# Optimization experiments

Hardware: AMD Instinct MI355X
Metric: run time of the kernel (lower is better)

## Reference

```python
import jax, jax.numpy as jnp
import numpy as np

B, N, P = 8, 64, 128
DNODE, DEDGE, DEMB = 2048, 1024, 512
E = B * N * N


def setup_inputs() -> dict:
    key = jax.random.key(0)
    ks = jax.random.split(key, 12)
    x = jax.random.normal(ks[0], (B, N, DNODE), dtype=jnp.float32)
    interaction_feature = jax.random.normal(ks[1], (B, N, N, DEDGE), dtype=jnp.float32)
    s = 0.02
    W_phi = jax.random.normal(ks[2], (DNODE, DEMB), dtype=jnp.float32) * s
    b_phi = jax.random.normal(ks[3], (DEMB,), dtype=jnp.float32) * s
    W_psi = jax.random.normal(ks[4], (DNODE, DEMB), dtype=jnp.float32) * s
    b_psi = jax.random.normal(ks[5], (DEMB,), dtype=jnp.float32) * s
    W_node = jax.random.normal(ks[6], (DNODE, DEMB), dtype=jnp.float32) * s
    b_node = jax.random.normal(ks[7], (DEMB,), dtype=jnp.float32) * s
    W_rel = jax.random.normal(ks[8], (DEDGE, DEMB), dtype=jnp.float32) * s
    b_rel = jax.random.normal(ks[9], (DEMB,), dtype=jnp.float32) * s
    pairs = jax.random.randint(ks[10], (B, P, 2), 0, N, dtype=jnp.int32)
    # edge_locating_tensor: rows (batch, src, dst) covering the proposed edge set
    bb, ii, jj = jnp.meshgrid(jnp.arange(B), jnp.arange(N), jnp.arange(N), indexing='ij')
    edge_locating_tensor = jnp.stack([bb.ravel(), ii.ravel(), jj.ravel()], axis=1).astype(jnp.int32)  # [E,3]
    return {"x": x, "interaction_feature": interaction_feature, "W_phi": W_phi, "b_phi": b_phi,
            "W_psi": W_psi, "b_psi": b_psi, "W_node": W_node, "b_node": b_node,
            "W_rel": W_rel, "b_rel": b_rel, "pairs": pairs, "edge_locating_tensor": edge_locating_tensor}


def _lookup_edge(elt, b_idx, i0, i1):
    # boolean-mask argmax lookup, faithful to torch argmax(loc0*loc1*loc2)
    # elt: [E,3]; b_idx,i0,i1: [B,P] -> loc: [B,P] indices into edge list
    m = (elt[None, None, :, 0] == b_idx[:, :, None]) \
        & (elt[None, None, :, 1] == i0[:, :, None]) \
        & (elt[None, None, :, 2] == i1[:, :, None])  # [B,P,E]
    return jnp.argmax(m, axis=-1)


def reference(x, interaction_feature, W_phi, b_phi, W_psi, b_psi,
              W_node, b_node, W_rel, b_rel, pairs, edge_locating_tensor):
    # relationship proposal scoring: all-pairs einsum + sigmoid
    phi = x @ W_phi + b_phi                                    # [B,N,512]
    psi = x @ W_psi + b_psi                                    # [B,N,512]
    relatedness_score = jax.nn.sigmoid(jnp.einsum('bik,bjk->bij', phi, psi))  # [B,N,N]

    # node / relationship-node embedders
    node_emb = x @ W_node + b_node                             # [B,N,512]
    elt = edge_locating_tensor
    rel_feats = interaction_feature[elt[:, 0], elt[:, 1], elt[:, 2]]  # [E,1024] gather
    edge_emb = rel_feats @ W_rel + b_rel                       # [E,512]

    # classifier input construction (gather/argmax/scatter hot path, vectorized)
    ind0, ind1 = pairs[..., 0], pairs[..., 1]                  # [B,P]
    b_idx = jnp.broadcast_to(jnp.arange(B, dtype=jnp.int32)[:, None], ind0.shape)
    emb0 = node_emb[b_idx, ind0]                               # [B,P,512]
    emb1 = node_emb[b_idx, ind1]
    first_half = (emb0 + emb1) * 0.5                           # aggregate 'mean'

    loc_fwd = _lookup_edge(elt, b_idx, ind0, ind1)             # [B,P]
    loc_rev = _lookup_edge(elt, b_idx, ind1, ind0)
    e1 = edge_emb[loc_fwd]                                     # [B,P,512]
    e2 = edge_emb[loc_rev]
    second_half = (e1 + e2) * 0.5

    classifier_input = jnp.concatenate([first_half, second_half], axis=-1)  # [B,P,1024]
    return relatedness_score, classifier_input
```

## Files before the change

### kernel.cpp

```cpp
#include <hip/hip_runtime.h>
#include <hip/hip_bf16.h>


typedef _Float16 h16;
typedef h16 h16x4 __attribute__((ext_vector_type(4)));
typedef h16 h16x8 __attribute__((ext_vector_type(8)));
typedef float f32x4 __attribute__((ext_vector_type(4)));

static const long O_W3T  = 0;
static const long O_WREL = 6291456;
static const long O_XH   = 7340032;
static const long O_G    = 9437184;
static const long O_B3   = 11534336;
static const long O_YH   = 11540480;

__global__ __launch_bounds__(256) void k_prep(
    const float* __restrict__ Wphi, const float* __restrict__ Wpsi,
    const float* __restrict__ Wnode, const float* __restrict__ Wrel,
    const float* __restrict__ x, const float* __restrict__ bphi,
    const float* __restrict__ bpsi, const float* __restrict__ bnode,
    const float* __restrict__ feat, const int* __restrict__ pairs,
    h16* __restrict__ W3t, h16* __restrict__ Wrelt, h16* __restrict__ xh,
    float* __restrict__ b3, h16* __restrict__ G) {
  __shared__ float t[32][33];
  int bid = blockIdx.x, tid = threadIdx.x;
  if (bid < 3584) {
    const float* src; h16* dst; int K, tk, tn;
    if (bid < 3072) {
      int mat = bid >> 10, rem = bid & 1023;
      tk = rem >> 4; tn = rem & 15;
      src = mat == 0 ? Wphi : (mat == 1 ? Wpsi : Wnode);
      K = 2048; dst = W3t + (long)mat * 512 * 2048;
    } else {
      int rem = bid - 3072;
      tk = rem >> 4; tn = rem & 15;
      src = Wrel; K = 1024; dst = Wrelt;
    }
    {
      int row = tid >> 3, c4 = (tid & 7) * 4;
      float4 v = *(const float4*)(src + (long)(tk*32 + row)*512 + tn*32 + c4);
      t[row][c4+0] = v.x; t[row][c4+1] = v.y; t[row][c4+2] = v.z; t[row][c4+3] = v.w;
    }
    __syncthreads();
    {
      int n = tid >> 3, k4 = (tid & 7) * 4;
      h16x4 o = { (h16)t[k4+0][n], (h16)t[k4+1][n], (h16)t[k4+2][n], (h16)t[k4+3][n] };
      *(h16x4*)(dst + (long)(tn*32 + n)*K + tk*32 + k4) = o;
    }
  } else if (bid < 4102) {
    int b2 = bid - 3584;
    if (b2 < 512) {
      int idx = (b2*256 + tid) * 8;
      const float4* xv = (const float4*)(x + idx);
      float4 v0 = xv[0], v1 = xv[1];
      h16x8 o;
      o[0]=(h16)v0.x; o[1]=(h16)v0.y; o[2]=(h16)v0.z; o[3]=(h16)v0.w;
      o[4]=(h16)v1.x; o[5]=(h16)v1.y; o[6]=(h16)v1.z; o[7]=(h16)v1.w;
      *(h16x8*)(xh + idx) = o;
    } else {
      int i = (b2 - 512)*256 + tid;
      if (i < 1536) b3[i] = i < 512 ? bphi[i] : (i < 1024 ? bpsi[i-512] : bnode[i-1024]);
    }
  } else {
    int r = bid - 4102;
    int b = r >> 7;
    int i0 = pairs[r*2], i1 = pairs[r*2+1];
    const float4* f0 = (const float4*)(feat + (long)((b*64 + i0)*64 + i1) * 1024);
    const float4* f1 = (const float4*)(feat + (long)((b*64 + i1)*64 + i0) * 1024);
    float4 a = f0[tid], c = f1[tid];
    h16x4 o;
    o[0]=(h16)(0.5f*(a.x+c.x)); o[1]=(h16)(0.5f*(a.y+c.y));
    o[2]=(h16)(0.5f*(a.z+c.z)); o[3]=(h16)(0.5f*(a.w+c.w));
    *(h16x4*)(G + (long)r*1024 + tid*4) = o;
  }
}

__device__ __forceinline__ void mfma4(
    const h16 (*__restrict__ As)[72], const h16 (*__restrict__ Bs)[72],
    int wm, int wn, int kb, int fr, f32x4 acc[2][2]) {
  h16x8 fa0 = *(const h16x8*)&As[wm*32 + fr][kb];
  h16x8 fa1 = *(const h16x8*)&As[wm*32 + 16 + fr][kb];
  h16x8 fb0 = *(const h16x8*)&Bs[wn*32 + fr][kb];
  h16x8 fb1 = *(const h16x8*)&Bs[wn*32 + 16 + fr][kb];
  acc[0][0] = __builtin_amdgcn_mfma_f32_16x16x32_f16(fa0, fb0, acc[0][0], 0,0,0);
  acc[0][1] = __builtin_amdgcn_mfma_f32_16x16x32_f16(fa0, fb1, acc[0][1], 0,0,0);
  acc[1][0] = __builtin_amdgcn_mfma_f32_16x16x32_f16(fa1, fb0, acc[1][0], 0,0,0);
  acc[1][1] = __builtin_amdgcn_mfma_f32_16x16x32_f16(fa1, fb1, acc[1][1], 0,0,0);
}

#define BAR_LDS() { asm volatile("s_waitcnt lgkmcnt(0)" ::: "memory"); \
                    __builtin_amdgcn_s_barrier(); }

template<int S>
__device__ __forceinline__ void tile_splitk(
    const h16* Agp, const h16* Bgp,
    h16 (*As)[64][72], h16 (*Bs)[64][72],
    int srow, int skp, int wm, int wn, int kb, int fr,
    f32x4 acc[2][2]) {
  h16x8 r0a = *(const h16x8*)(Agp);
  h16x8 r0b = *(const h16x8*)(Bgp);
  *(h16x8*)&As[0][srow][skp] = r0a;
  *(h16x8*)&Bs[0][srow][skp] = r0b;
  h16x8 ra1 = *(const h16x8*)(Agp + 64),  rb1 = *(const h16x8*)(Bgp + 64);
  h16x8 ra2 = *(const h16x8*)(Agp + 128), rb2 = *(const h16x8*)(Bgp + 128);
  BAR_LDS();
  int cur = 0;
#pragma unroll 1
  for (int k0 = 192; k0 < S * 64; k0 += 64) {
    h16x8 raF = *(const h16x8*)(Agp + k0);
    h16x8 rbF = *(const h16x8*)(Bgp + k0);
    mfma4(As[cur], Bs[cur], wm, wn, kb, fr, acc);
    *(h16x8*)&As[cur ^ 1][srow][skp] = ra1;
    *(h16x8*)&Bs[cur ^ 1][srow][skp] = rb1;
    BAR_LDS();
    ra1 = ra2; rb1 = rb2; ra2 = raF; rb2 = rbF;
    cur ^= 1;
  }
  mfma4(As[cur], Bs[cur], wm, wn, kb, fr, acc);
  *(h16x8*)&As[cur ^ 1][srow][skp] = ra1;
  *(h16x8*)&Bs[cur ^ 1][srow][skp] = rb1;
  BAR_LDS();
  cur ^= 1;
  mfma4(As[cur], Bs[cur], wm, wn, kb, fr, acc);
  *(h16x8*)&As[cur ^ 1][srow][skp] = ra2;
  *(h16x8*)&Bs[cur ^ 1][srow][skp] = rb2;
  BAR_LDS();
  cur ^= 1;
  mfma4(As[cur], Bs[cur], wm, wn, kb, fr, acc);
}

__device__ __forceinline__ void splitk_merge(
    h16 (*As)[64][72], int wave, int lane, f32x4 acc[2][2]) {
  float* mb = (float*)As;
  __syncthreads();
  if (wave >= 4) {
    int mi = ((wave - 4) * 64 + lane) * 16;
    *(f32x4*)&mb[mi +  0] = acc[0][0];
    *(f32x4*)&mb[mi +  4] = acc[0][1];
    *(f32x4*)&mb[mi +  8] = acc[1][0];
    *(f32x4*)&mb[mi + 12] = acc[1][1];
  }
  __syncthreads();
  if (wave < 4) {
    int mi = (wave * 64 + lane) * 16;
    acc[0][0] += *(const f32x4*)&mb[mi +  0];
    acc[0][1] += *(const f32x4*)&mb[mi +  4];
    acc[1][0] += *(const f32x4*)&mb[mi +  8];
    acc[1][1] += *(const f32x4*)&mb[mi + 12];
  }
}

__global__ __launch_bounds__(512) void k_gemm(
    const h16* __restrict__ xh, const h16* __restrict__ W3t,
    const float* __restrict__ b3, h16* __restrict__ Yh,
    const h16* __restrict__ G, const h16* __restrict__ Wrelt,
    const float* __restrict__ brel, float* __restrict__ out) {
  __shared__ __align__(16) h16 As[2][64][72];
  __shared__ __align__(16) h16 Bs[2][64][72];
  int bid = blockIdx.x, tid = threadIdx.x;
  int lane = tid & 63, wave = tid >> 6;
  int kslice = wave >> 2, wsub = wave & 3;
  int wm = wsub >> 1, wn = wsub & 1;
  int srow = tid >> 3, skp = (tid & 7) * 8;
  int fr = lane & 15, kb = kslice * 32 + (lane >> 4) * 8;
  int r0 = 4 * (lane >> 4), c0 = lane & 15;

  int isEdge = bid >= 192;
  int ntile = isEdge ? 2 : 1;
#pragma unroll 1
  for (int ti = 0; ti < ntile; ++ti) {
    if (ti) __syncthreads();
    const h16 *A, *Bt; int K, tileM, tileN;
    if (!isEdge) {
      A = xh; Bt = W3t; K = 2048;
      tileM = (bid / 24) * 64; tileN = (bid % 24) * 64;
    } else {
      int e = (bid - 192) * 2 + ti;
      A = G; Bt = Wrelt; K = 1024;
      tileM = (e >> 3) * 64; tileN = (e & 7) * 64;
    }
    const h16* Agp = A + (long)(tileM + srow) * K + skp;
    const h16* Bgp = Bt + (long)(tileN + srow) * K + skp;
    f32x4 acc[2][2] = {};
    if (!isEdge) tile_splitk<32>(Agp, Bgp, As, Bs, srow, skp, wm, wn, kb, fr, acc);
    else         tile_splitk<16>(Agp, Bgp, As, Bs, srow, skp, wm, wn, kb, fr, acc);
    splitk_merge(As, wave, lane, acc);

    if (wave < 4) {
#pragma unroll
      for (int m = 0; m < 2; ++m)
#pragma unroll
        for (int n = 0; n < 2; ++n) {
          int row = tileM + wm*32 + m*16 + r0;
          int col = tileN + wn*32 + n*16 + c0;
          if (!isEdge) {
            float bb = b3[col];
#pragma unroll
            for (int r = 0; r < 4; ++r)
              Yh[(long)(row + r) * 1536 + col] = (h16)(acc[m][n][r] + bb);
          } else {
            float bb = brel[col];
#pragma unroll
            for (int r = 0; r < 4; ++r)
              out[32768 + 512 + (long)(row + r) * 1024 + col] = acc[m][n][r] + bb;
          }
        }
    }
  }
}

__global__ __launch_bounds__(512) void k_epilogue(
    const h16* __restrict__ Yh, const int* __restrict__ pairs,
    float* __restrict__ out) {
  __shared__ __align__(16) h16 As[2][64][72];
  __shared__ __align__(16) h16 Bs[2][64][72];
  int bid = blockIdx.x, tid = threadIdx.x;
  if (bid < 8) {
    int lane = tid & 63, wave = tid >> 6;
    int kslice = wave >> 2, wsub = wave & 3;
    int wm = wsub >> 1, wn = wsub & 1;
    int srow = tid >> 3, skp = (tid & 7) * 8;
    int fr = lane & 15, kb = kslice * 32 + (lane >> 4) * 8;
    const h16* Ab = Yh + (long)bid * 64 * 1536;
    const h16* Agp = Ab + (long)srow * 1536 + skp;
    const h16* Bgp = Ab + (long)srow * 1536 + 512 + skp;
    f32x4 acc[2][2] = {};
    tile_splitk<8>(Agp, Bgp, As, Bs, srow, skp, wm, wn, kb, fr, acc);
    splitk_merge(As, wave, lane, acc);
    if (wave < 4) {
      int r0 = 4 * (lane >> 4), c0 = lane & 15;
      float* ob = out + (long)bid * 4096;
#pragma unroll
      for (int m = 0; m < 2; ++m)
#pragma unroll
        for (int n = 0; n < 2; ++n) {
          int row = wm*32 + m*16 + r0;
          int col = wn*32 + n*16 + c0;
#pragma unroll
          for (int r = 0; r < 4; ++r) {
            float s = acc[m][n][r];
            ob[(long)(row + r) * 64 + col] = 1.f / (1.f + expf(-s));
          }
        }
    }
  } else {
    int r = bid - 8;
    int b = r >> 7;
    int i0 = pairs[r*2], i1 = pairs[r*2+1];
    const h16* n0 = Yh + (long)(b*64 + i0)*1536 + 1024;
    const h16* n1 = Yh + (long)(b*64 + i1)*1536 + 1024;
    float* o = out + 32768 + (long)r*1024;
    if (tid < 512)
      o[tid] = 0.5f*((float)n0[tid] + (float)n1[tid]);
  }
}

extern "C" void kernel_launch(void* const* d_in, const int* in_sizes, int n_in,
                              void* d_out, int out_size, void* d_ws, size_t ws_size,
                              hipStream_t stream) {
  const float* x     = (const float*)d_in[0];
  const float* feat  = (const float*)d_in[1];
  const float* Wphi  = (const float*)d_in[2];
  const float* bphi  = (const float*)d_in[3];
  const float* Wpsi  = (const float*)d_in[4];
  const float* bpsi  = (const float*)d_in[5];
  const float* Wnode = (const float*)d_in[6];
  const float* bnode = (const float*)d_in[7];
  const float* Wrel  = (const float*)d_in[8];
  const float* brel  = (const float*)d_in[9];
  const int*   pairs = (const int*)d_in[10];
  float* out = (float*)d_out;
  char* ws = (char*)d_ws;

  h16*   W3t   = (h16*)(ws + O_W3T);
  h16*   Wrelt = (h16*)(ws + O_WREL);
  h16*   xh    = (h16*)(ws + O_XH);
  h16*   G     = (h16*)(ws + O_G);
  float* b3    = (float*)(ws + O_B3);
  h16*   Yh    = (h16*)(ws + O_YH);

  k_prep<<<dim3(5126), dim3(256), 0, stream>>>(
      Wphi, Wpsi, Wnode, Wrel, x, bphi, bpsi, bnode, feat, pairs,
      W3t, Wrelt, xh, b3, G);
  k_gemm<<<dim3(256), dim3(512), 0, stream>>>(
      xh, W3t, b3, Yh, G, Wrelt, brel, out);
  k_epilogue<<<dim3(1032), dim3(512), 0, stream>>>(Yh, pairs, out);
}
```

Baseline: 33.79 us.

## Replace split-K 64x64 GEMM tiles with 128x128 tiles without split-K

The fused GEMM kernel now uses 128x128 output tiles with eight waves, each computing a 64x32 sub-block over the full K range, instead of 64x64 tiles with a two-way split-K and an LDS merge. This raises data reuse per loaded tile, removes the split-K merge and its barriers, and cuts the grid from 256 blocks to 80. The cost is far fewer blocks than the GPU's compute units, so parallelism drops, along with more dynamic LDS per block. The redundant tid<512 guard in the epilogue is also dropped.

New measurement: 43.72 us. +29.4%, slower.

```diff
diff --git a/kernel.cpp b/kernel.cpp
--- a/kernel.cpp
+++ b/kernel.cpp
@@ -75,6 +75,125 @@
   }
 }
 
+#define BAR_LDS() { asm volatile("s_waitcnt lgkmcnt(0)" ::: "memory"); \
+                    __builtin_amdgcn_s_barrier(); }
+
+__device__ __forceinline__ void mfma8(
+    const h16 (*__restrict__ As)[72], const h16 (*__restrict__ Bs)[72],
+    int wm, int wn, int fr, int kg, f32x4 acc[4][2]) {
+#pragma unroll
+  for (int kc = 0; kc < 2; ++kc) {
+    int kb = kc*32 + kg;
+    h16x8 fb0 = *(const h16x8*)&Bs[wn*32 + fr][kb];
+    h16x8 fb1 = *(const h16x8*)&Bs[wn*32 + 16 + fr][kb];
+#pragma unroll
+    for (int i = 0; i < 4; ++i) {
+      h16x8 fa = *(const h16x8*)&As[wm*64 + i*16 + fr][kb];
+      acc[i][0] = __builtin_amdgcn_mfma_f32_16x16x32_f16(fa, fb0, acc[i][0], 0,0,0);
+      acc[i][1] = __builtin_amdgcn_mfma_f32_16x16x32_f16(fa, fb1, acc[i][1], 0,0,0);
+    }
+  }
+}
+
+template<int S>
+__device__ __forceinline__ void tile128(
+    const h16* Agp, const h16* Bgp,
+    h16 (*As)[128][72], h16 (*Bs)[128][72],
+    int srow, int skp, int wm, int wn, int fr, int kg,
+    f32x4 acc[4][2]) {
+  h16x8 a0 = *(const h16x8*)(Agp),      a0b = *(const h16x8*)(Agp + 8);
+  h16x8 b0 = *(const h16x8*)(Bgp),      b0b = *(const h16x8*)(Bgp + 8);
+  *(h16x8*)&As[0][srow][skp]     = a0;
+  *(h16x8*)&As[0][srow][skp + 8] = a0b;
+  *(h16x8*)&Bs[0][srow][skp]     = b0;
+  *(h16x8*)&Bs[0][srow][skp + 8] = b0b;
+  h16x8 a1  = *(const h16x8*)(Agp + 64),      a1b = *(const h16x8*)(Agp + 72);
+  h16x8 b1  = *(const h16x8*)(Bgp + 64),      b1b = *(const h16x8*)(Bgp + 72);
+  h16x8 a2  = *(const h16x8*)(Agp + 128),     a2b = *(const h16x8*)(Agp + 136);
+  h16x8 b2  = *(const h16x8*)(Bgp + 128),     b2b = *(const h16x8*)(Bgp + 136);
+  BAR_LDS();
+  int cur = 0;
+#pragma unroll 1
+  for (int k0 = 192; k0 < S * 64; k0 += 64) {
+    h16x8 aF  = *(const h16x8*)(Agp + k0),     aFb = *(const h16x8*)(Agp + k0 + 8);
+    h16x8 bF  = *(const h16x8*)(Bgp + k0),     bFb = *(const h16x8*)(Bgp + k0 + 8);
+    mfma8(As[cur], Bs[cur], wm, wn, fr, kg, acc);
+    *(h16x8*)&As[cur ^ 1][srow][skp]     = a1;
+    *(h16x8*)&As[cur ^ 1][srow][skp + 8] = a1b;
+    *(h16x8*)&Bs[cur ^ 1][srow][skp]     = b1;
+    *(h16x8*)&Bs[cur ^ 1][srow][skp + 8] = b1b;
+    BAR_LDS();
+    a1 = a2; a1b = a2b; b1 = b2; b1b = b2b;
+    a2 = aF; a2b = aFb; b2 = bF; b2b = bFb;
+    cur ^= 1;
+  }
+  mfma8(As[cur], Bs[cur], wm, wn, fr, kg, acc);
+  *(h16x8*)&As[cur ^ 1][srow][skp]     = a1;
+  *(h16x8*)&As[cur ^ 1][srow][skp + 8] = a1b;
+  *(h16x8*)&Bs[cur ^ 1][srow][skp]     = b1;
+  *(h16x8*)&Bs[cur ^ 1][srow][skp + 8] = b1b;
+  BAR_LDS();
+  cur ^= 1;
+  mfma8(As[cur], Bs[cur], wm, wn, fr, kg, acc);
+  *(h16x8*)&As[cur ^ 1][srow][skp]     = a2;
+  *(h16x8*)&As[cur ^ 1][srow][skp + 8] = a2b;
+  *(h16x8*)&Bs[cur ^ 1][srow][skp]     = b2;
+  *(h16x8*)&Bs[cur ^ 1][srow][skp + 8] = b2b;
+  BAR_LDS();
+  cur ^= 1;
+  mfma8(As[cur], Bs[cur], wm, wn, fr, kg, acc);
+}
+
+__global__ __launch_bounds__(512) void k_gemm(
+    const h16* __restrict__ xh, const h16* __restrict__ W3t,
+    const float* __restrict__ b3, h16* __restrict__ Yh,
+    const h16* __restrict__ G, const h16* __restrict__ Wrelt,
+    const float* __restrict__ brel, float* __restrict__ out) {
+  extern __shared__ __align__(16) h16 ldsbuf[];
+  h16 (*As)[128][72] = (h16 (*)[128][72])ldsbuf;
+  h16 (*Bs)[128][72] = (h16 (*)[128][72])(ldsbuf + 18432);
+  int bid = blockIdx.x, tid = threadIdx.x;
+  int lane = tid & 63, wave = tid >> 6;
+  int wm = wave >> 2, wn = wave & 3;
+  int srow = tid >> 2, skp = (tid & 3) * 16;
+  int fr = lane & 15, kg = (lane >> 4) * 8;
+  int r0 = 4 * (lane >> 4), c0 = lane & 15;
+
+  const h16 *A, *Bt; int K, tileM, tileN, S;
+  if (bid < 48) {
+    A = xh; Bt = W3t; K = 2048; S = 32;
+    tileM = (bid / 12) * 128; tileN = (bid % 12) * 128;
+  } else {
+    int e = bid - 48;
+    A = G; Bt = Wrelt; K = 1024; S = 16;
+    tileM = (e >> 2) * 128; tileN = (e & 3) * 128;
+  }
+  const h16* Agp = A + (long)(tileM + srow) * K + skp;
+  const h16* Bgp = Bt + (long)(tileN + srow) * K + skp;
+  f32x4 acc[4][2] = {};
+  if (S == 32) tile128<32>(Agp, Bgp, As, Bs, srow, skp, wm, wn, fr, kg, acc);
+  else         tile128<16>(Agp, Bgp, As, Bs, srow, skp, wm, wn, fr, kg, acc);
+
+#pragma unroll
+  for (int m = 0; m < 4; ++m)
+#pragma unroll
+    for (int n = 0; n < 2; ++n) {
+      int row = tileM + wm*64 + m*16 + r0;
+      int col = tileN + wn*32 + n*16 + c0;
+      if (bid < 48) {
+        float bb = b3[col];
+#pragma unroll
+        for (int r = 0; r < 4; ++r)
+          Yh[(long)(row + r) * 1536 + col] = (h16)(acc[m][n][r] + bb);
+      } else {
+        float bb = brel[col];
+#pragma unroll
+        for (int r = 0; r < 4; ++r)
+          out[32768 + 512 + (long)(row + r) * 1024 + col] = acc[m][n][r] + bb;
+      }
+    }
+}
+
 __device__ __forceinline__ void mfma4(
     const h16 (*__restrict__ As)[72], const h16 (*__restrict__ Bs)[72],
     int wm, int wn, int kb, int fr, f32x4 acc[2][2]) {
@@ -87,9 +206,6 @@
   acc[1][0] = __builtin_amdgcn_mfma_f32_16x16x32_f16(fa1, fb0, acc[1][0], 0,0,0);
   acc[1][1] = __builtin_amdgcn_mfma_f32_16x16x32_f16(fa1, fb1, acc[1][1], 0,0,0);
 }
-
-#define BAR_LDS() { asm volatile("s_waitcnt lgkmcnt(0)" ::: "memory"); \
-                    __builtin_amdgcn_s_barrier(); }
 
 template<int S>
 __device__ __forceinline__ void tile_splitk(
@@ -147,65 +263,6 @@
     acc[0][1] += *(const f32x4*)&mb[mi +  4];
     acc[1][0] += *(const f32x4*)&mb[mi +  8];
     acc[1][1] += *(const f32x4*)&mb[mi + 12];
-  }
-}
-
-__global__ __launch_bounds__(512) void k_gemm(
-    const h16* __restrict__ xh, const h16* __restrict__ W3t,
-    const float* __restrict__ b3, h16* __restrict__ Yh,
-    const h16* __restrict__ G, const h16* __restrict__ Wrelt,
-    const float* __restrict__ brel, float* __restrict__ out) {
-  __shared__ __align__(16) h16 As[2][64][72];
-  __shared__ __align__(16) h16 Bs[2][64][72];
-  int bid = blockIdx.x, tid = threadIdx.x;
-  int lane = tid & 63, wave = tid >> 6;
-  int kslice = wave >> 2, wsub = wave & 3;
-  int wm = wsub >> 1, wn = wsub & 1;
-  int srow = tid >> 3, skp = (tid & 7) * 8;
-  int fr = lane & 15, kb = kslice * 32 + (lane >> 4) * 8;
-  int r0 = 4 * (lane >> 4), c0 = lane & 15;
-
-  int isEdge = bid >= 192;
-  int ntile = isEdge ? 2 : 1;
-#pragma unroll 1
-  for (int ti = 0; ti < ntile; ++ti) {
-    if (ti) __syncthreads();
-    const h16 *A, *Bt; int K, tileM, tileN;
-    if (!isEdge) {
-      A = xh; Bt = W3t; K = 2048;
-      tileM = (bid / 24) * 64; tileN = (bid % 24) * 64;
-    } else {
-      int e = (bid - 192) * 2 + ti;
-      A = G; Bt = Wrelt; K = 1024;
-      tileM = (e >> 3) * 64; tileN = (e & 7) * 64;
-    }
-    const h16* Agp = A + (long)(tileM + srow) * K + skp;
-    const h16* Bgp = Bt + (long)(tileN + srow) * K + skp;
-    f32x4 acc[2][2] = {};
-    if (!isEdge) tile_splitk<32>(Agp, Bgp, As, Bs, srow, skp, wm, wn, kb, fr, acc);
-    else         tile_splitk<16>(Agp, Bgp, As, Bs, srow, skp, wm, wn, kb, fr, acc);
-    splitk_merge(As, wave, lane, acc);
-
-    if (wave < 4) {
-#pragma unroll
-      for (int m = 0; m < 2; ++m)
-#pragma unroll
-        for (int n = 0; n < 2; ++n) {
-          int row = tileM + wm*32 + m*16 + r0;
-          int col = tileN + wn*32 + n*16 + c0;
-          if (!isEdge) {
-            float bb = b3[col];
-#pragma unroll
-            for (int r = 0; r < 4; ++r)
-              Yh[(long)(row + r) * 1536 + col] = (h16)(acc[m][n][r] + bb);
-          } else {
-            float bb = brel[col];
-#pragma unroll
-            for (int r = 0; r < 4; ++r)
-              out[32768 + 512 + (long)(row + r) * 1024 + col] = acc[m][n][r] + bb;
-          }
-        }
-    }
   }
 }
 
@@ -250,8 +307,7 @@
     const h16* n0 = Yh + (long)(b*64 + i0)*1536 + 1024;
     const h16* n1 = Yh + (long)(b*64 + i1)*1536 + 1024;
     float* o = out + 32768 + (long)r*1024;
-    if (tid < 512)
-      o[tid] = 0.5f*((float)n0[tid] + (float)n1[tid]);
+    o[tid] = 0.5f*((float)n0[tid] + (float)n1[tid]);
   }
 }
 
@@ -279,10 +335,13 @@
   float* b3    = (float*)(ws + O_B3);
   h16*   Yh    = (h16*)(ws + O_YH);
 
+  hipFuncSetAttribute((const void*)k_gemm,
+                      hipFuncAttributeMaxDynamicSharedMemorySize, 73728);
+
   k_prep<<<dim3(5126), dim3(256), 0, stream>>>(
       Wphi, Wpsi, Wnode, Wrel, x, bphi, bpsi, bnode, feat, pairs,
       W3t, Wrelt, xh, b3, G);
-  k_gemm<<<dim3(256), dim3(512), 0, stream>>>(
+  k_gemm<<<dim3(80), dim3(512), 73728, stream>>>(
       xh, W3t, b3, Yh, G, Wrelt, brel, out);
   k_epilogue<<<dim3(1032), dim3(512), 0, stream>>>(Yh, pairs, out);
 }
```
